# Kernel optimization log

Measured on AMD Instinct MI355X. Metric: run time of the kernel, lower is better.

Reference implementation:

```python
import jax, jax.numpy as jnp
import numpy as np

N_NODES = 50000
N_EDGES = 800000
F_IN = 64
HID = 64
N_CLASSES = 10
N_GRAPHS = 64


def setup_inputs() -> dict:
    key = jax.random.key(0)
    ks = jax.random.split(key, 16)
    x = jax.random.normal(ks[0], (N_NODES, F_IN), dtype=jnp.float32)
    edge_index = jax.random.randint(ks[1], (2, N_EDGES), 0, N_NODES, dtype=jnp.int32)
    supernode_mask = jax.random.bernoulli(ks[2], 0.1, (N_NODES,))
    edge_mask = jax.random.bernoulli(ks[3], 0.5, (N_EDGES,)).astype(jnp.float32)
    batch = jnp.sort(jax.random.randint(ks[4], (N_NODES,), 0, N_GRAPHS, dtype=jnp.int32))
    def glorot(k, fan_in, fan_out):
        s = jnp.sqrt(6.0 / (fan_in + fan_out))
        return jax.random.uniform(k, (fan_in, fan_out), jnp.float32, -s, s)
    W1 = glorot(ks[5], F_IN, HID); b1 = jnp.zeros((HID,), jnp.float32)
    W2 = glorot(ks[6], HID, HID); b2 = jnp.zeros((HID,), jnp.float32)
    W3 = glorot(ks[7], HID, HID); b3 = jnp.zeros((HID,), jnp.float32)
    Wl = glorot(ks[8], HID, N_CLASSES); bl = jnp.zeros((N_CLASSES,), jnp.float32)
    return {"x": x, "edge_index": edge_index, "supernode_mask": supernode_mask,
            "edge_mask": edge_mask, "batch": batch,
            "W1": W1, "b1": b1, "W2": W2, "b2": b2, "W3": W3, "b3": b3,
            "Wl": Wl, "bl": bl}


def reference(x, edge_index, supernode_mask, edge_mask, batch,
              W1, b1, W2, b2, W3, b3, Wl, bl):
    N = x.shape[0]
    src, dst = edge_index[0], edge_index[1]

    # SimpleConv('add'): weighted sum of source features into targets
    x2 = jax.ops.segment_sum(x[src] * edge_mask[:, None], dst, num_segments=N)
    x = jnp.where(supernode_mask[:, None], x2, x)

    # GCN normalization with self-loops: deg = 1 + in-degree, norm = d^-1/2[src]*d^-1/2[dst]
    deg = jax.ops.segment_sum(jnp.ones((src.shape[0],), x.dtype), dst, num_segments=N) + 1.0
    dinv = jax.lax.rsqrt(deg)
    coef = dinv[src] * dinv[dst]          # [E]
    self_coef = (dinv * dinv)[:, None]    # self-loop contribution [N,1]

    def gcn(h, W, b):
        h = h @ W  # small GEMM [N, HID]
        agg = jax.ops.segment_sum(h[src] * coef[:, None], dst, num_segments=N)
        return agg + h * self_coef + b

    h = jax.nn.relu(gcn(x, W1, b1))
    h = jax.nn.relu(gcn(h, W2, b2))
    h = gcn(h, W3, b3)

    # global_mean_pool over graphs
    sums = jax.ops.segment_sum(h, batch, num_segments=N_GRAPHS)
    cnt = jax.ops.segment_sum(jnp.ones((N,), h.dtype), batch, num_segments=N_GRAPHS)
    pooled = sums / jnp.maximum(cnt, 1.0)[:, None]

    # dropout is identity in eval mode
    return pooled @ Wl + bl
```

## Files before the change

### kernel.cpp

```cpp
#include <hip/hip_runtime.h>

#define FEAT 64
#define NGRAPH 64
#define POOL_CHUNKS 8

typedef short bf16x8 __attribute__((ext_vector_type(8)));
typedef float f32x4 __attribute__((ext_vector_type(4)));
union FragU { uint4 u4; bf16x8 h; };


__device__ __forceinline__ unsigned int pack_bf16(float a, float b) {
    unsigned int ua = __float_as_uint(a), ub = __float_as_uint(b);
    ua = (ua + 0x7FFFu + ((ua >> 16) & 1u)) >> 16;
    ub = (ub + 0x7FFFu + ((ub >> 16) & 1u)) >> 16;
    return ua | (ub << 16);
}
__device__ __forceinline__ float bf_lo(unsigned int w) {
    return __uint_as_float(w << 16);
}
__device__ __forceinline__ float bf_hi(unsigned int w) {
    return __uint_as_float(w & 0xFFFF0000u);
}

__global__ __launch_bounds__(256) void k_init(int* __restrict__ cnt_int,
                                              float* __restrict__ pooled,
                                              int* __restrict__ flag, int N) {
    int i = blockIdx.x * 256 + threadIdx.x;
    if (i < N) cnt_int[i] = 0;
    if (i < NGRAPH * FEAT) pooled[i] = 0.f;
    if (i == 0) *flag = 0;
}

__global__ __launch_bounds__(256) void k_wcvt(const float* __restrict__ W1,
                                              const float* __restrict__ W2,
                                              const float* __restrict__ W3,
                                              unsigned int* __restrict__ wt) {
    int t = blockIdx.x * 256 + threadIdx.x;
    if (t >= 3 * 2048) return;
    int m = t >> 11, w = t & 2047;
    int c = w >> 5, kw = w & 31;
    const float* W = (m == 0) ? W1 : ((m == 1) ? W2 : W3);
    wt[t] = pack_bf16(W[(2 * kw) * 64 + c], W[(2 * kw + 1) * 64 + c]);
}

__global__ __launch_bounds__(256) void k_detect(const unsigned int* __restrict__ m,
                                                int nwords, int* __restrict__ flag) {
    int i = blockIdx.x * 256 + threadIdx.x;
    if (i >= nwords) return;
    unsigned int w = m[i];
    if (w == 0x3F800000u) atomicOr(flag, 2);
    else if (w > 1u) atomicOr(flag, 1);
}

__device__ __forceinline__ bool read_mask(const void* sm, int i, int fl) {
    if (fl & 2) return ((const float*)sm)[i] != 0.f;
    if (fl & 1) return ((const unsigned char*)sm)[i] != 0;
    return ((const int*)sm)[i] != 0;
}

__global__ __launch_bounds__(256) void k_count(const int* __restrict__ ei,
                                               int* __restrict__ cnt_int,
                                               int* __restrict__ rank, int E) {
    int e = blockIdx.x * 256 + threadIdx.x;
    if (e >= E) return;
    rank[e] = atomicAdd(&cnt_int[ei[E + e]], 1);
}

__global__ __launch_bounds__(256) void k_scan1(const int* __restrict__ cnt,
                                               int* __restrict__ rowptr,
                                               int* __restrict__ bsum, int N) {
    __shared__ int woff[4];
    int t = threadIdx.x, lane = t & 63, wid = t >> 6;
    int i = blockIdx.x * 256 + t;
    int orig = (i < N) ? cnt[i] : 0;
    int v = orig;
#pragma unroll
    for (int off = 1; off < 64; off <<= 1) {
        int u = __shfl_up(v, off);
        if (lane >= off) v += u;
    }
    if (lane == 63) woff[wid] = v;
    __syncthreads();
    if (t == 0) {
        int a = 0;
#pragma unroll
        for (int w = 0; w < 4; ++w) { int b = woff[w]; woff[w] = a; a += b; }
    }
    __syncthreads();
    int excl = woff[wid] + v - orig;
    if (i < N) rowptr[i] = excl;
    if (t == 255) bsum[blockIdx.x] = woff[3] + v;
}

__global__ __launch_bounds__(256) void k_scan2(int* __restrict__ bsum, int nb) {
    __shared__ int woff[4];
    int t = threadIdx.x, lane = t & 63, wid = t >> 6;
    int orig = (t < nb) ? bsum[t] : 0;
    int v = orig;
#pragma unroll
    for (int off = 1; off < 64; off <<= 1) {
        int u = __shfl_up(v, off);
        if (lane >= off) v += u;
    }
    if (lane == 63) woff[wid] = v;
    __syncthreads();
    if (t == 0) {
        int a = 0;
#pragma unroll
        for (int w = 0; w < 4; ++w) { int b = woff[w]; woff[w] = a; a += b; }
    }
    __syncthreads();
    if (t < nb) bsum[t] = woff[wid] + v - orig;
}

__global__ __launch_bounds__(256) void k_scan3(const int* __restrict__ cnt,
                                               const int* __restrict__ bsum,
                                               int* __restrict__ rowptr,
                                               float* __restrict__ dinv,
                                               int N, int E) {
    int i = blockIdx.x * 256 + threadIdx.x;
    if (i >= N) return;
    rowptr[i] += bsum[blockIdx.x];
    dinv[i] = rsqrtf((float)cnt[i] + 1.0f);
    if (i == 0) rowptr[N] = E;
}

__global__ __launch_bounds__(256) void k_fill(const int* __restrict__ ei,
                                              const float* __restrict__ emask,
                                              const int* __restrict__ rowptr,
                                              const int* __restrict__ rank,
                                              unsigned int* __restrict__ csr, int E) {
    int e = blockIdx.x * 256 + threadIdx.x;
    if (e >= E) return;
    int dst = ei[E + e];
    unsigned int word = (unsigned int)ei[e];
    if (emask[e] != 0.f) word |= 0x10000u;
    csr[rowptr[dst] + rank[e]] = word;
}

__global__ __launch_bounds__(256) void k_sup(const float* __restrict__ x,
                                             const int* __restrict__ rowptr,
                                             const unsigned int* __restrict__ csr,
                                             const void* __restrict__ sm,
                                             const int* __restrict__ flag,
                                             unsigned int* __restrict__ u, int N) {
    int t = blockIdx.x * 256 + threadIdx.x;
    int i = t >> 6, lane = t & 63;
    if (i >= N) return;
    int g = lane >> 4, q = lane & 15;
    int fl = *flag;
    float4 acc;
    if (read_mask(sm, i, fl)) {
        int r0 = rowptr[i], r1 = rowptr[i + 1];
        acc.x = 0.f; acc.y = 0.f; acc.z = 0.f; acc.w = 0.f;
        for (int j0 = r0; j0 < r1; j0 += 64) {
            int cnt = min(64, r1 - j0);
            unsigned int w_l = (lane < cnt) ? csr[j0 + lane] : 0u;
            int rounds4 = (cnt + 3) & ~3;
#pragma unroll 2
            for (int j = 0; j < rounds4; j += 4) {
                unsigned int wd = __shfl(w_l, j + g);
                if (wd & 0x10000u) {
                    int s = (int)(wd & 0xFFFFu);
                    const float4 v = *(const float4*)(x + (size_t)s * FEAT + q * 4);
                    acc.x += v.x; acc.y += v.y; acc.z += v.z; acc.w += v.w;
                }
            }
        }
#pragma unroll
        for (int m = 16; m < 64; m <<= 1) {
            acc.x += __shfl_xor(acc.x, m);
            acc.y += __shfl_xor(acc.y, m);
            acc.z += __shfl_xor(acc.z, m);
            acc.w += __shfl_xor(acc.w, m);
        }
    } else {
        acc = *(const float4*)(x + (size_t)i * FEAT + q * 4);
    }
    if (g == 0) {
        uint2 p;
        p.x = pack_bf16(acc.x, acc.y);
        p.y = pack_bf16(acc.z, acc.w);
        *(uint2*)(u + (size_t)i * 32 + q * 2) = p;
    }
}

__global__ __launch_bounds__(256) void k_gemm_mfma(const unsigned int* __restrict__ u_in,
                                                   const unsigned int* __restrict__ wbfT,
                                                   const float* __restrict__ dinv,
                                                   unsigned int* __restrict__ hd, int N) {
    int wid = threadIdx.x >> 6, lane = threadIdx.x & 63;
    int row0 = (blockIdx.x * 4 + wid) * 16;
    if (row0 >= N) return;
    int r = lane & 15, half = lane >> 4;
    f32x4 acc0 = {0.f, 0.f, 0.f, 0.f}, acc1 = acc0, acc2 = acc0, acc3 = acc0;
#pragma unroll
    for (int ks = 0; ks < 2; ++ks) {
        FragU a;
        a.u4 = *(const uint4*)(u_in + (size_t)(row0 + r) * 32 + ks * 16 + half * 4);
        FragU b0, b1, b2, b3;
        b0.u4 = *(const uint4*)(wbfT + (0 * 16 + r) * 32 + ks * 16 + half * 4);
        b1.u4 = *(const uint4*)(wbfT + (1 * 16 + r) * 32 + ks * 16 + half * 4);
        b2.u4 = *(const uint4*)(wbfT + (2 * 16 + r) * 32 + ks * 16 + half * 4);
        b3.u4 = *(const uint4*)(wbfT + (3 * 16 + r) * 32 + ks * 16 + half * 4);
        acc0 = __builtin_amdgcn_mfma_f32_16x16x32_bf16(a.h, b0.h, acc0, 0, 0, 0);
        acc1 = __builtin_amdgcn_mfma_f32_16x16x32_bf16(a.h, b1.h, acc1, 0, 0, 0);
        acc2 = __builtin_amdgcn_mfma_f32_16x16x32_bf16(a.h, b2.h, acc2, 0, 0, 0);
        acc3 = __builtin_amdgcn_mfma_f32_16x16x32_bf16(a.h, b3.h, acc3, 0, 0, 0);
    }
    float dd0 = dinv[row0 + half * 4 + 0];
    float dd1 = dinv[row0 + half * 4 + 1];
    float dd2 = dinv[row0 + half * 4 + 2];
    float dd3 = dinv[row0 + half * 4 + 3];
#pragma unroll
    for (int t = 0; t < 4; ++t) {
        const f32x4 acc = (t == 0) ? acc0 : (t == 1) ? acc1 : (t == 2) ? acc2 : acc3;
        float v0 = acc[0] * dd0, v1 = acc[1] * dd1, v2 = acc[2] * dd2, v3 = acc[3] * dd3;
        float o0 = __shfl_xor(v0, 1), o1 = __shfl_xor(v1, 1),
              o2 = __shfl_xor(v2, 1), o3 = __shfl_xor(v3, 1);
        if ((r & 1) == 0) {
            size_t base = (size_t)(row0 + half * 4) * 32 + t * 8 + (r >> 1);
            hd[base + 0 * 32] = pack_bf16(v0, o0);
            hd[base + 1 * 32] = pack_bf16(v1, o1);
            hd[base + 2 * 32] = pack_bf16(v2, o2);
            hd[base + 3 * 32] = pack_bf16(v3, o3);
        }
    }
}

__global__ __launch_bounds__(256) void k_gather(const unsigned int* __restrict__ hd,
                                                const float* __restrict__ b,
                                                const float* __restrict__ dinv,
                                                const int* __restrict__ rowptr,
                                                const unsigned int* __restrict__ csr,
                                                unsigned int* __restrict__ u_out,
                                                float* __restrict__ h_out,
                                                int N, int mode) {
    int t = blockIdx.x * 256 + threadIdx.x;
    int i = t >> 6, lane = t & 63;
    if (i >= N) return;
    int g = lane >> 4, q = lane & 15;
    int r0 = rowptr[i], r1 = rowptr[i + 1];
    float4 acc = {0.f, 0.f, 0.f, 0.f};
    for (int j0 = r0; j0 < r1; j0 += 64) {
        int cnt = min(64, r1 - j0);
        int s_l = (lane < cnt) ? (int)(csr[j0 + lane] & 0xFFFFu) : 0;
        int rounds4 = (cnt + 3) & ~3;
#pragma unroll 4
        for (int j = 0; j < rounds4; j += 4) {
            int jj = j + g;
            int s = __shfl(s_l, jj);
            if (jj < cnt) {
                const uint2 v = *(const uint2*)(hd + (size_t)s * 32 + q * 2);
                acc.x += bf_lo(v.x); acc.y += bf_hi(v.x);
                acc.z += bf_lo(v.y); acc.w += bf_hi(v.y);
            }
        }
    }
#pragma unroll
    for (int m = 16; m < 64; m <<= 1) {
        acc.x += __shfl_xor(acc.x, m);
        acc.y += __shfl_xor(acc.y, m);
        acc.z += __shfl_xor(acc.z, m);
        acc.w += __shfl_xor(acc.w, m);
    }
    if (g == 0) {
        float dd = dinv[i];
        const uint2 hv = *(const uint2*)(hd + (size_t)i * 32 + q * 2);
        const float4 bv = *(const float4*)(b + q * 4);
        float4 r;
        r.x = (acc.x + bf_lo(hv.x)) * dd + bv.x;
        r.y = (acc.y + bf_hi(hv.x)) * dd + bv.y;
        r.z = (acc.z + bf_lo(hv.y)) * dd + bv.z;
        r.w = (acc.w + bf_hi(hv.y)) * dd + bv.w;
        if (mode == 0) {
            r.x = fmaxf(r.x, 0.f); r.y = fmaxf(r.y, 0.f);
            r.z = fmaxf(r.z, 0.f); r.w = fmaxf(r.w, 0.f);
            uint2 p;
            p.x = pack_bf16(r.x, r.y);
            p.y = pack_bf16(r.z, r.w);
            *(uint2*)(u_out + (size_t)i * 32 + q * 2) = p;
        } else {
            *(float4*)(h_out + (size_t)i * FEAT + q * 4) = r;
        }
    }
}

__device__ __forceinline__ int lbound(const int* a, int n, int key) {
    int lo = 0, hi = n;
    while (lo < hi) {
        int mid = (lo + hi) >> 1;
        if (a[mid] < key) lo = mid + 1; else hi = mid;
    }
    return lo;
}

__global__ __launch_bounds__(256) void k_pool(const float* __restrict__ xbuf,
                                              const int* __restrict__ batch,
                                              float* __restrict__ pooled,
                                              float* __restrict__ gcnt, int N) {
    int g = blockIdx.x >> 3, c = blockIdx.x & (POOL_CHUNKS - 1);
    int lo = lbound(batch, N, g);
    int hi = lbound(batch, N, g + 1);
    int len = hi - lo;
    int t = threadIdx.x, lane = t & 63, sub = t >> 6;
    if (c == 0 && t == 0) gcnt[g] = (float)len;
    int a = lo + (int)(((long long)len * c) / POOL_CHUNKS);
    int bnd = lo + (int)(((long long)len * (c + 1)) / POOL_CHUNKS);
    float s = 0.f;
    for (int i = a + sub; i < bnd; i += 4) s += xbuf[(size_t)i * FEAT + lane];
    __shared__ float red[4][64];
    red[sub][lane] = s;
    __syncthreads();
    if (sub == 0) {
        float tot = red[0][lane] + red[1][lane] + red[2][lane] + red[3][lane];
        unsafeAtomicAdd(&pooled[g * FEAT + lane], tot);
    }
}

__global__ __launch_bounds__(640) void k_logits(const float* __restrict__ pooled,
                                                const float* __restrict__ gcnt,
                                                const float* __restrict__ Wl,
                                                const float* __restrict__ bl,
                                                float* __restrict__ out) {
    int t = threadIdx.x;
    if (t >= NGRAPH * 10) return;
    int g = t / 10, cls = t % 10;
    float inv = 1.f / fmaxf(gcnt[g], 1.f);
    float s = 0.f;
#pragma unroll
    for (int f = 0; f < 64; ++f) s += pooled[g * 64 + f] * Wl[f * 10 + cls];
    out[t] = s * inv + bl[cls];
}

extern "C" void kernel_launch(void* const* d_in, const int* in_sizes, int n_in,
                              void* d_out, int out_size, void* d_ws, size_t ws_size,
                              hipStream_t stream) {
    const float* x = (const float*)d_in[0];
    const int* ei = (const int*)d_in[1];
    const void* sm = d_in[2];
    const float* emask = (const float*)d_in[3];
    const int* batch = (const int*)d_in[4];
    const float* W1 = (const float*)d_in[5];
    const float* b1 = (const float*)d_in[6];
    const float* W2 = (const float*)d_in[7];
    const float* b2 = (const float*)d_in[8];
    const float* W3 = (const float*)d_in[9];
    const float* b3 = (const float*)d_in[10];
    const float* Wl = (const float*)d_in[11];
    const float* bl = (const float*)d_in[12];

    const int N = in_sizes[0] / FEAT;
    const int E = in_sizes[1] / 2;

    float* wsf = (float*)d_ws;
    size_t off = 0;
    float* xbuf = wsf + off;          off += (size_t)N * FEAT;
    unsigned int* ua = (unsigned int*)(wsf + off); off += (size_t)N * 32;
    unsigned int* ub = (unsigned int*)(wsf + off); off += (size_t)N * 32;
    unsigned int* hd = (unsigned int*)(wsf + off); off += (size_t)N * 32;
    unsigned int* wbf = (unsigned int*)(wsf + off); off += 3 * 2048;
    int* rowptr = (int*)(wsf + off);  off += N + 1;
    int* rank = (int*)(wsf + off);    off += E;
    int* cnt_int = (int*)(wsf + off); off += N;
    float* dinv = wsf + off;          off += N;
    int* bsum = (int*)(wsf + off);    off += 256;
    unsigned int* csr = (unsigned int*)(wsf + off); off += E;
    float* pooled = wsf + off;        off += NGRAPH * FEAT;
    float* gcnt = wsf + off;          off += NGRAPH;
    int* flag = (int*)(wsf + off);

    const int nblocks = (N + 255) / 256;
    const int eblocks = (E + 255) / 256;
    const int wblocks = (N * 64 + 255) / 256;
    const int gemm_blocks = (N / 16 + 3) / 4;
    const int detect_blocks = (N / 4 + 255) / 256;

    k_init<<<nblocks, 256, 0, stream>>>(cnt_int, pooled, flag, N);
    k_wcvt<<<24, 256, 0, stream>>>(W1, W2, W3, wbf);
    k_detect<<<detect_blocks, 256, 0, stream>>>((const unsigned int*)sm, N / 4, flag);
    k_count<<<eblocks, 256, 0, stream>>>(ei, cnt_int, rank, E);
    k_scan1<<<nblocks, 256, 0, stream>>>(cnt_int, rowptr, bsum, N);
    k_scan2<<<1, 256, 0, stream>>>(bsum, nblocks);
    k_scan3<<<nblocks, 256, 0, stream>>>(cnt_int, bsum, rowptr, dinv, N, E);
    k_fill<<<eblocks, 256, 0, stream>>>(ei, emask, rowptr, rank, csr, E);
    k_sup<<<wblocks, 256, 0, stream>>>(x, rowptr, csr, sm, flag, ua, N);

    k_gemm_mfma<<<gemm_blocks, 256, 0, stream>>>(ua, wbf + 0 * 2048, dinv, hd, N);
    k_gather<<<wblocks, 256, 0, stream>>>(hd, b1, dinv, rowptr, csr, ub, (float*)nullptr, N, 0);
    k_gemm_mfma<<<gemm_blocks, 256, 0, stream>>>(ub, wbf + 1 * 2048, dinv, hd, N);
    k_gather<<<wblocks, 256, 0, stream>>>(hd, b2, dinv, rowptr, csr, ua, (float*)nullptr, N, 0);
    k_gemm_mfma<<<gemm_blocks, 256, 0, stream>>>(ua, wbf + 2 * 2048, dinv, hd, N);
    k_gather<<<wblocks, 256, 0, stream>>>(hd, b3, dinv, rowptr, csr, (unsigned int*)nullptr, xbuf, N, 1);

    k_pool<<<NGRAPH * POOL_CHUNKS, 256, 0, stream>>>(xbuf, batch, pooled, gcnt, N);
    k_logits<<<1, 640, 0, stream>>>(pooled, gcnt, Wl, bl, (float*)d_out);
}
```

Measured before the change: 215.5 us.

## Widen gather loads, skip non-supernode waves, store final layer in bf16

A new bulk bf16 conversion kernel writes x into the feature buffer, so k_sup now returns early for non-supernode rows and only gathers for the roughly 10% of nodes that are supernodes. k_gather switches from 4 neighbours per round with 8-byte loads to 8 neighbours per round with 16-byte loads, which halves the number of gather rounds. The last layer's output is kept in bf16 rather than fp32, and k_pool reads bf16 directly, cutting its read traffic. In exchange this adds one kernel launch, and rounding the final features to bf16 slightly changes numerics.

```diff
diff --git a/kernel.cpp b/kernel.cpp
--- a/kernel.cpp
+++ b/kernel.cpp
@@ -41,6 +41,20 @@
     int c = w >> 5, kw = w & 31;
     const float* W = (m == 0) ? W1 : ((m == 1) ? W2 : W3);
     wt[t] = pack_bf16(W[(2 * kw) * 64 + c], W[(2 * kw + 1) * 64 + c]);
+}
+
+__global__ __launch_bounds__(256) void k_xcvt(const float* __restrict__ x,
+                                              unsigned int* __restrict__ u, int n8) {
+    int t = blockIdx.x * 256 + threadIdx.x;
+    if (t >= n8) return;
+    const float4 a = *(const float4*)(x + (size_t)t * 8);
+    const float4 b = *(const float4*)(x + (size_t)t * 8 + 4);
+    uint4 p;
+    p.x = pack_bf16(a.x, a.y);
+    p.y = pack_bf16(a.z, a.w);
+    p.z = pack_bf16(b.x, b.y);
+    p.w = pack_bf16(b.z, b.w);
+    *(uint4*)(u + (size_t)t * 4) = p;
 }
 
 __global__ __launch_bounds__(256) void k_detect(const unsigned int* __restrict__ m,
@@ -147,35 +161,31 @@
     int t = blockIdx.x * 256 + threadIdx.x;
     int i = t >> 6, lane = t & 63;
     if (i >= N) return;
+    int fl = *flag;
+    if (!read_mask(sm, i, fl)) return;
     int g = lane >> 4, q = lane & 15;
-    int fl = *flag;
-    float4 acc;
-    if (read_mask(sm, i, fl)) {
-        int r0 = rowptr[i], r1 = rowptr[i + 1];
-        acc.x = 0.f; acc.y = 0.f; acc.z = 0.f; acc.w = 0.f;
-        for (int j0 = r0; j0 < r1; j0 += 64) {
-            int cnt = min(64, r1 - j0);
-            unsigned int w_l = (lane < cnt) ? csr[j0 + lane] : 0u;
-            int rounds4 = (cnt + 3) & ~3;
+    int r0 = rowptr[i], r1 = rowptr[i + 1];
+    float4 acc = {0.f, 0.f, 0.f, 0.f};
+    for (int j0 = r0; j0 < r1; j0 += 64) {
+        int cnt = min(64, r1 - j0);
+        unsigned int w_l = (lane < cnt) ? csr[j0 + lane] : 0u;
+        int rounds4 = (cnt + 3) & ~3;
 #pragma unroll 2
-            for (int j = 0; j < rounds4; j += 4) {
-                unsigned int wd = __shfl(w_l, j + g);
-                if (wd & 0x10000u) {
-                    int s = (int)(wd & 0xFFFFu);
-                    const float4 v = *(const float4*)(x + (size_t)s * FEAT + q * 4);
-                    acc.x += v.x; acc.y += v.y; acc.z += v.z; acc.w += v.w;
-                }
+        for (int j = 0; j < rounds4; j += 4) {
+            unsigned int wd = __shfl(w_l, j + g);
+            if (wd & 0x10000u) {
+                int s = (int)(wd & 0xFFFFu);
+                const float4 v = *(const float4*)(x + (size_t)s * FEAT + q * 4);
+                acc.x += v.x; acc.y += v.y; acc.z += v.z; acc.w += v.w;
             }
         }
-#pragma unroll
-        for (int m = 16; m < 64; m <<= 1) {
-            acc.x += __shfl_xor(acc.x, m);
-            acc.y += __shfl_xor(acc.y, m);
-            acc.z += __shfl_xor(acc.z, m);
-            acc.w += __shfl_xor(acc.w, m);
-        }
-    } else {
-        acc = *(const float4*)(x + (size_t)i * FEAT + q * 4);
+    }
+#pragma unroll
+    for (int m = 16; m < 64; m <<= 1) {
+        acc.x += __shfl_xor(acc.x, m);
+        acc.y += __shfl_xor(acc.y, m);
+        acc.z += __shfl_xor(acc.z, m);
+        acc.w += __shfl_xor(acc.w, m);
     }
     if (g == 0) {
         uint2 p;
@@ -234,55 +244,59 @@
                                                 const int* __restrict__ rowptr,
                                                 const unsigned int* __restrict__ csr,
                                                 unsigned int* __restrict__ u_out,
-                                                float* __restrict__ h_out,
-                                                int N, int mode) {
+                                                int N, int do_relu) {
     int t = blockIdx.x * 256 + threadIdx.x;
     int i = t >> 6, lane = t & 63;
     if (i >= N) return;
-    int g = lane >> 4, q = lane & 15;
+    int g = lane >> 3, q = lane & 7;
     int r0 = rowptr[i], r1 = rowptr[i + 1];
-    float4 acc = {0.f, 0.f, 0.f, 0.f};
+    float acc[8] = {0.f, 0.f, 0.f, 0.f, 0.f, 0.f, 0.f, 0.f};
     for (int j0 = r0; j0 < r1; j0 += 64) {
         int cnt = min(64, r1 - j0);
         int s_l = (lane < cnt) ? (int)(csr[j0 + lane] & 0xFFFFu) : 0;
-        int rounds4 = (cnt + 3) & ~3;
-#pragma unroll 4
-        for (int j = 0; j < rounds4; j += 4) {
+        int rounds8 = (cnt + 7) & ~7;
+#pragma unroll 2
+        for (int j = 0; j < rounds8; j += 8) {
             int jj = j + g;
             int s = __shfl(s_l, jj);
             if (jj < cnt) {
-                const uint2 v = *(const uint2*)(hd + (size_t)s * 32 + q * 2);
-                acc.x += bf_lo(v.x); acc.y += bf_hi(v.x);
-                acc.z += bf_lo(v.y); acc.w += bf_hi(v.y);
+                const uint4 v = *(const uint4*)(hd + (size_t)s * 32 + q * 4);
+                acc[0] += bf_lo(v.x); acc[1] += bf_hi(v.x);
+                acc[2] += bf_lo(v.y); acc[3] += bf_hi(v.y);
+                acc[4] += bf_lo(v.z); acc[5] += bf_hi(v.z);
+                acc[6] += bf_lo(v.w); acc[7] += bf_hi(v.w);
             }
         }
     }
 #pragma unroll
-    for (int m = 16; m < 64; m <<= 1) {
-        acc.x += __shfl_xor(acc.x, m);
-        acc.y += __shfl_xor(acc.y, m);
-        acc.z += __shfl_xor(acc.z, m);
-        acc.w += __shfl_xor(acc.w, m);
+    for (int m = 8; m < 64; m <<= 1) {
+#pragma unroll
+        for (int k = 0; k < 8; ++k) acc[k] += __shfl_xor(acc[k], m);
     }
     if (g == 0) {
         float dd = dinv[i];
-        const uint2 hv = *(const uint2*)(hd + (size_t)i * 32 + q * 2);
-        const float4 bv = *(const float4*)(b + q * 4);
-        float4 r;
-        r.x = (acc.x + bf_lo(hv.x)) * dd + bv.x;
-        r.y = (acc.y + bf_hi(hv.x)) * dd + bv.y;
-        r.z = (acc.z + bf_lo(hv.y)) * dd + bv.z;
-        r.w = (acc.w + bf_hi(hv.y)) * dd + bv.w;
-        if (mode == 0) {
-            r.x = fmaxf(r.x, 0.f); r.y = fmaxf(r.y, 0.f);
-            r.z = fmaxf(r.z, 0.f); r.w = fmaxf(r.w, 0.f);
-            uint2 p;
-            p.x = pack_bf16(r.x, r.y);
-            p.y = pack_bf16(r.z, r.w);
-            *(uint2*)(u_out + (size_t)i * 32 + q * 2) = p;
-        } else {
-            *(float4*)(h_out + (size_t)i * FEAT + q * 4) = r;
+        const uint4 hv = *(const uint4*)(hd + (size_t)i * 32 + q * 4);
+        const float4 b0 = *(const float4*)(b + q * 8);
+        const float4 b1 = *(const float4*)(b + q * 8 + 4);
+        float r[8];
+        r[0] = (acc[0] + bf_lo(hv.x)) * dd + b0.x;
+        r[1] = (acc[1] + bf_hi(hv.x)) * dd + b0.y;
+        r[2] = (acc[2] + bf_lo(hv.y)) * dd + b0.z;
+        r[3] = (acc[3] + bf_hi(hv.y)) * dd + b0.w;
+        r[4] = (acc[4] + bf_lo(hv.z)) * dd + b1.x;
+        r[5] = (acc[5] + bf_hi(hv.z)) * dd + b1.y;
+        r[6] = (acc[6] + bf_lo(hv.w)) * dd + b1.z;
+        r[7] = (acc[7] + bf_hi(hv.w)) * dd + b1.w;
+        if (do_relu) {
+#pragma unroll
+            for (int k = 0; k < 8; ++k) r[k] = fmaxf(r[k], 0.f);
         }
+        uint4 p;
+        p.x = pack_bf16(r[0], r[1]);
+        p.y = pack_bf16(r[2], r[3]);
+        p.z = pack_bf16(r[4], r[5]);
+        p.w = pack_bf16(r[6], r[7]);
+        *(uint4*)(u_out + (size_t)i * 32 + q * 4) = p;
     }
 }
 
@@ -295,7 +309,7 @@
     return lo;
 }
 
-__global__ __launch_bounds__(256) void k_pool(const float* __restrict__ xbuf,
+__global__ __launch_bounds__(256) void k_pool(const unsigned int* __restrict__ xb,
                                               const int* __restrict__ batch,
                                               float* __restrict__ pooled,
                                               float* __restrict__ gcnt, int N) {
@@ -308,7 +322,12 @@
     int a = lo + (int)(((long long)len * c) / POOL_CHUNKS);
     int bnd = lo + (int)(((long long)len * (c + 1)) / POOL_CHUNKS);
     float s = 0.f;
-    for (int i = a + sub; i < bnd; i += 4) s += xbuf[(size_t)i * FEAT + lane];
+    int w = lane >> 1;
+    bool hi_half = lane & 1;
+    for (int i = a + sub; i < bnd; i += 4) {
+        unsigned int word = xb[(size_t)i * 32 + w];
+        s += hi_half ? bf_hi(word) : bf_lo(word);
+    }
     __shared__ float red[4][64];
     red[sub][lane] = s;
     __syncthreads();
@@ -355,7 +374,6 @@
 
     float* wsf = (float*)d_ws;
     size_t off = 0;
-    float* xbuf = wsf + off;          off += (size_t)N * FEAT;
     unsigned int* ua = (unsigned int*)(wsf + off); off += (size_t)N * 32;
     unsigned int* ub = (unsigned int*)(wsf + off); off += (size_t)N * 32;
     unsigned int* hd = (unsigned int*)(wsf + off); off += (size_t)N * 32;
@@ -375,9 +393,11 @@
     const int wblocks = (N * 64 + 255) / 256;
     const int gemm_blocks = (N / 16 + 3) / 4;
     const int detect_blocks = (N / 4 + 255) / 256;
+    const int xcvt_blocks = (N * 8 + 255) / 256;
 
     k_init<<<nblocks, 256, 0, stream>>>(cnt_int, pooled, flag, N);
     k_wcvt<<<24, 256, 0, stream>>>(W1, W2, W3, wbf);
+    k_xcvt<<<xcvt_blocks, 256, 0, stream>>>(x, ua, N * 8);
     k_detect<<<detect_blocks, 256, 0, stream>>>((const unsigned int*)sm, N / 4, flag);
     k_count<<<eblocks, 256, 0, stream>>>(ei, cnt_int, rank, E);
     k_scan1<<<nblocks, 256, 0, stream>>>(cnt_int, rowptr, bsum, N);
@@ -387,12 +407,12 @@
     k_sup<<<wblocks, 256, 0, stream>>>(x, rowptr, csr, sm, flag, ua, N);
 
     k_gemm_mfma<<<gemm_blocks, 256, 0, stream>>>(ua, wbf + 0 * 2048, dinv, hd, N);
-    k_gather<<<wblocks, 256, 0, stream>>>(hd, b1, dinv, rowptr, csr, ub, (float*)nullptr, N, 0);
+    k_gather<<<wblocks, 256, 0, stream>>>(hd, b1, dinv, rowptr, csr, ub, N, 1);
     k_gemm_mfma<<<gemm_blocks, 256, 0, stream>>>(ub, wbf + 1 * 2048, dinv, hd, N);
-    k_gather<<<wblocks, 256, 0, stream>>>(hd, b2, dinv, rowptr, csr, ua, (float*)nullptr, N, 0);
+    k_gather<<<wblocks, 256, 0, stream>>>(hd, b2, dinv, rowptr, csr, ua, N, 1);
     k_gemm_mfma<<<gemm_blocks, 256, 0, stream>>>(ua, wbf + 2 * 2048, dinv, hd, N);
-    k_gather<<<wblocks, 256, 0, stream>>>(hd, b3, dinv, rowptr, csr, (unsigned int*)nullptr, xbuf, N, 1);
-
-    k_pool<<<NGRAPH * POOL_CHUNKS, 256, 0, stream>>>(xbuf, batch, pooled, gcnt, N);
+    k_gather<<<wblocks, 256, 0, stream>>>(hd, b3, dinv, rowptr, csr, ub, N, 0);
+
+    k_pool<<<NGRAPH * POOL_CHUNKS, 256, 0, stream>>>(ub, batch, pooled, gcnt, N);
     k_logits<<<1, 640, 0, stream>>>(pooled, gcnt, Wl, bl, (float*)d_out);
 }
```

Measured after the change: 210.1 us. -2.5%, faster.
